# Performance work log

Measured on AMD Instinct MI355X. Metric: run time of the kernel, lower is better.

Reference implementation:

```python
import jax, jax.numpy as jnp
import numpy as np

B, N, H = 8, 2048, 256

def setup_inputs() -> dict:
    key = jax.random.key(0)
    k1, k2, k3, k4, k5 = jax.random.split(key, 5)
    h = jax.random.normal(k1, (B, N, H), dtype=jnp.float32)
    node_mask = jnp.ones((B, N, 1), dtype=jnp.float32)
    n_nodes = N  # unused by the forward math, kept for signature fidelity
    s1 = 1.0 / np.sqrt(H)
    W1 = jax.random.uniform(k2, (H, H), minval=-s1, maxval=s1, dtype=jnp.float32)
    b1 = jax.random.uniform(k3, (H,), minval=-s1, maxval=s1, dtype=jnp.float32)
    w2 = jax.random.uniform(k4, (H,), minval=-s1, maxval=s1, dtype=jnp.float32)
    b2 = jax.random.uniform(k5, (), minval=-s1, maxval=s1, dtype=jnp.float32)
    return {"h": h, "node_mask": node_mask, "n_nodes": n_nodes,
            "W1": W1, "b1": b1, "w2": w2, "b2": b2}

def reference(h, node_mask, n_nodes, W1, b1, w2, b2):
    # node_dec: Linear + SiLU
    x = jax.nn.silu(jnp.einsum('bnh,oh->bno', h, W1) + b1)  # [B,N,H]
    # pre_di applied to pairwise difference is linear, so factor:
    # pre_di(x_i - x_j) = (x_i @ w2) - (x_j @ w2) + b2
    s = jnp.einsum('bnh,h->bn', x, w2)                       # [B,N]
    out = s[:, :, None] - s[:, None, :] + b2                 # [B,N,N]
    return out.astype(jnp.int64)                             # torch .long() truncates
```

## Files before the change

kernel.cpp:

```cpp
#include <hip/hip_runtime.h>
#include <math.h>

#define B_ 8
#define N_ 2048
#define H_ 256

typedef double d4 __attribute__((ext_vector_type(4)));

__global__ __launch_bounds__(256)
void transpose_w1(const float* __restrict__ W1, float* __restrict__ W1T) {
    W1T[(size_t)blockIdx.x * H_ + threadIdx.x] =
        W1[(size_t)threadIdx.x * H_ + blockIdx.x];
}

__device__ __forceinline__ int self_probe_var() {
    const int l = threadIdx.x & 63;
    d4 z = {0.0, 0.0, 0.0, 0.0};
    d4 r1 = __builtin_amdgcn_mfma_f64_16x16x4f64((double)(l + 1), 1.0, z, 0, 0, 0);
    d4 r2 = __builtin_amdgcn_mfma_f64_16x16x4f64(1.0, (double)(l + 1), z, 0, 0, 0);
    d4 r3 = __builtin_amdgcn_mfma_f64_16x16x4f64((double)(l & 15), 1.0, z, 0, 0, 0);
    const double pw0 = __shfl(r1[0], 0, 64);
    const double pw1 = __shfl(r2[0], 0, 64);
    const double pw2 = __shfl(r3[0], 1, 64);
    const double pw3 = __shfl(r3[2], 16, 64);
    const double pw4 = __shfl(r2[2], 16, 64);
    if (pw0 != 100.0 || pw1 != 100.0) return 0;
    if (pw2 == 0.0 && pw3 == 24.0)  return 1;
    if (pw2 == 0.0 && pw3 == 36.0)  return 3;
    if (pw2 == 4.0 && pw4 == 124.0) return 2;
    if (pw2 == 4.0 && pw4 == 136.0) return 4;
    return 0;
}

__global__ __launch_bounds__(256)
__attribute__((amdgpu_waves_per_eu(2, 4)))
void s_mfma_uni(const float* __restrict__ hp, const float* __restrict__ W1T,
                const float* __restrict__ b1, const float* __restrict__ w2,
                double* __restrict__ s_out) {
    const int var = self_probe_var();
    if (var == 0) return;
    __shared__ float hs_t[H_][17];
    __shared__ double spart[4][16];
    const int t = threadIdx.x;
    const int lane = t & 63;
    const int wave = __builtin_amdgcn_readfirstlane(t >> 6);
    const int a15 = lane & 15, g = lane >> 4;
    const int m0 = blockIdx.x * 16;
    const int oc = wave * 64;

    #pragma unroll
    for (int i = 0; i < 16; ++i)
        hs_t[t][i] = hp[(size_t)(m0 + i) * H_ + t];
    __syncthreads();

    const float* bp = W1T + (size_t)g * H_ + oc + a15;

    d4 acc[4];
    #pragma unroll
    for (int ot = 0; ot < 4; ++ot) acc[ot] = (d4){0.0, 0.0, 0.0, 0.0};

    float ac[2], an[2];
    float bcv[8], bnv[8];
    ac[0] = hs_t[g][a15];
    ac[1] = hs_t[4 + g][a15];
    #pragma unroll
    for (int ot = 0; ot < 4; ++ot) {
        bcv[ot]     = bp[ot * 16];
        bcv[4 + ot] = bp[4 * H_ + ot * 16];
    }

    for (int kc = 0; kc < H_; kc += 8) {
        const int kn = (kc + 8 < H_) ? (kc + 8) : 0;
        an[0] = hs_t[kn + g][a15];
        an[1] = hs_t[kn + 4 + g][a15];
        #pragma unroll
        for (int ot = 0; ot < 4; ++ot) {
            bnv[ot]     = bp[(size_t)kn * H_ + ot * 16];
            bnv[4 + ot] = bp[(size_t)(kn + 4) * H_ + ot * 16];
        }
        {
            const double a0 = (double)ac[0];
            #pragma unroll
            for (int ot = 0; ot < 4; ++ot)
                acc[ot] = __builtin_amdgcn_mfma_f64_16x16x4f64(
                    a0, (double)bcv[ot], acc[ot], 0, 0, 0);
        }
        {
            const double a1 = (double)ac[1];
            #pragma unroll
            for (int ot = 0; ot < 4; ++ot)
                acc[ot] = __builtin_amdgcn_mfma_f64_16x16x4f64(
                    a1, (double)bcv[4 + ot], acc[ot], 0, 0, 0);
        }
        ac[0] = an[0]; ac[1] = an[1];
        #pragma unroll
        for (int q = 0; q < 8; ++q) bcv[q] = bnv[q];
    }

    if (var == 1 || var == 3) {
        double psum[4] = {0.0, 0.0, 0.0, 0.0};
        #pragma unroll
        for (int ot = 0; ot < 4; ++ot) {
            const int o = oc + ot * 16 + a15;
            const double bb = (double)b1[o];
            const double ww = (double)w2[o];
            #pragma unroll
            for (int v = 0; v < 4; ++v) {
                const double u = acc[ot][v] + bb;
                psum[v] += ww * (u / (1.0 + exp(-u)));
            }
        }
        #pragma unroll
        for (int v = 0; v < 4; ++v) {
            double x = psum[v];
            x += __shfl_xor(x, 1, 64);
            x += __shfl_xor(x, 2, 64);
            x += __shfl_xor(x, 4, 64);
            x += __shfl_xor(x, 8, 64);
            psum[v] = x;
        }
        if (a15 == 0) {
            #pragma unroll
            for (int v = 0; v < 4; ++v) {
                const int row = (var == 1) ? (4 * g + v) : (g + 4 * v);
                spart[wave][row] = psum[v];
            }
        }
    } else {
        double ps = 0.0;
        #pragma unroll
        for (int ot = 0; ot < 4; ++ot)
            #pragma unroll
            for (int v = 0; v < 4; ++v) {
                const int cv = (var == 2) ? (4 * g + v) : (g + 4 * v);
                const int o = oc + ot * 16 + cv;
                const double u = acc[ot][v] + (double)b1[o];
                ps += (double)w2[o] * (u / (1.0 + exp(-u)));
            }
        ps += __shfl_xor(ps, 16, 64);
        ps += __shfl_xor(ps, 32, 64);
        if (g == 0) spart[wave][a15] = ps;
    }
    __syncthreads();
    if (t < 16)
        s_out[m0 + t] = spart[0][t] + spart[1][t] + spart[2][t] + spart[3][t];
}

__global__ __launch_bounds__(256)
__attribute__((amdgpu_waves_per_eu(2, 4)))
void s_valu_kernel(const float* __restrict__ hp, const float* __restrict__ W1T,
                   const float* __restrict__ b1, const float* __restrict__ w2,
                   double* __restrict__ s_out) {
    if (self_probe_var() != 0) return;
    const int t = threadIdx.x;
    const int lane = t & 63;
    const int wave = __builtin_amdgcn_readfirstlane(t >> 6);
    const int m0 = blockIdx.x * 16 + wave * 4;
    const int o0 = lane * 4;
    const float* hr = hp + (size_t)m0 * H_;
    const float* wp = W1T + o0;

    double acc[4][4];
    #pragma unroll
    for (int j = 0; j < 4; ++j)
        #pragma unroll
        for (int r = 0; r < 4; ++r) acc[j][r] = 0.0;

    float4 wA[8], wB[8];
    float hA[32], hB[32];

    #define LOADW(dst, kcv)                                                   \
        do {                                                                  \
            _Pragma("unroll")                                                 \
            for (int kk = 0; kk < 8; ++kk)                                    \
                dst[kk] = *reinterpret_cast<const float4*>(                   \
                    wp + (size_t)((kcv) + kk) * H_);                          \
        } while (0)

    #define LOADH(dst, kcv)                                                   \
        do {                                                                  \
            _Pragma("unroll")                                                 \
            for (int r = 0; r < 4; ++r)                                       \
                _Pragma("unroll")                                             \
                for (int kk = 0; kk < 8; ++kk)                                \
                    dst[r * 8 + kk] = hr[r * H_ + (kcv) + kk];                \
        } while (0)

    #define COMPUTE(wv, hbuf)                                                 \
        do {                                                                  \
            _Pragma("unroll")                                                 \
            for (int kk = 0; kk < 8; ++kk) {                                  \
                const double h0 = (double)hbuf[0 * 8 + kk];                   \
                const double h1 = (double)hbuf[1 * 8 + kk];                   \
                const double h2 = (double)hbuf[2 * 8 + kk];                   \
                const double h3 = (double)hbuf[3 * 8 + kk];                   \
                const double a0 = (double)wv[kk].x;                           \
                const double a1 = (double)wv[kk].y;                           \
                const double a2 = (double)wv[kk].z;                           \
                const double a3 = (double)wv[kk].w;                           \
                acc[0][0] = fma(a0, h0, acc[0][0]);                           \
                acc[0][1] = fma(a0, h1, acc[0][1]);                           \
                acc[0][2] = fma(a0, h2, acc[0][2]);                           \
                acc[0][3] = fma(a0, h3, acc[0][3]);                           \
                acc[1][0] = fma(a1, h0, acc[1][0]);                           \
                acc[1][1] = fma(a1, h1, acc[1][1]);                           \
                acc[1][2] = fma(a1, h2, acc[1][2]);                           \
                acc[1][3] = fma(a1, h3, acc[1][3]);                           \
                acc[2][0] = fma(a2, h0, acc[2][0]);                           \
                acc[2][1] = fma(a2, h1, acc[2][1]);                           \
                acc[2][2] = fma(a2, h2, acc[2][2]);                           \
                acc[2][3] = fma(a2, h3, acc[2][3]);                           \
                acc[3][0] = fma(a3, h0, acc[3][0]);                           \
                acc[3][1] = fma(a3, h1, acc[3][1]);                           \
                acc[3][2] = fma(a3, h2, acc[3][2]);                           \
                acc[3][3] = fma(a3, h3, acc[3][3]);                           \
            }                                                                 \
        } while (0)

    LOADW(wA, 0);
    LOADH(hA, 0);
    for (int kc = 0; kc < H_; kc += 16) {
        LOADW(wB, kc + 8);
        LOADH(hB, kc + 8);
        COMPUTE(wA, hA);
        if (kc + 16 < H_) {
            LOADW(wA, kc + 16);
            LOADH(hA, kc + 16);
        }
        COMPUTE(wB, hB);
    }
    #undef LOADW
    #undef LOADH
    #undef COMPUTE

    const float4 b1v = *reinterpret_cast<const float4*>(b1 + o0);
    const float4 w2v = *reinterpret_cast<const float4*>(w2 + o0);
    double psum[4] = {0.0, 0.0, 0.0, 0.0};
    #define EPI(j, bc, wc)                                                    \
        do {                                                                  \
            const double bb = (double)bc, ww = (double)wc;                    \
            _Pragma("unroll")                                                 \
            for (int r = 0; r < 4; ++r) {                                     \
                const double u = acc[j][r] + bb;                              \
                psum[r] += ww * (u / (1.0 + exp(-u)));                        \
            }                                                                 \
        } while (0)
    EPI(0, b1v.x, w2v.x);
    EPI(1, b1v.y, w2v.y);
    EPI(2, b1v.z, w2v.z);
    EPI(3, b1v.w, w2v.w);
    #undef EPI

    #pragma unroll
    for (int r = 0; r < 4; ++r) {
        double v = psum[r];
        v += __shfl_xor(v, 1, 64);
        v += __shfl_xor(v, 2, 64);
        v += __shfl_xor(v, 4, 64);
        v += __shfl_xor(v, 8, 64);
        v += __shfl_xor(v, 16, 64);
        v += __shfl_xor(v, 32, 64);
        if (lane == 0) s_out[m0 + r] = v;
    }
}

__global__ __launch_bounds__(256)
void pair_kernel(const double* __restrict__ s, const float* __restrict__ b2p,
                 int* __restrict__ out) {
    const double b2 = (double)b2p[0];
    const unsigned total4 = (unsigned)(B_) * (unsigned)(N_) * (unsigned)(N_) / 4u;
    const unsigned stride = gridDim.x * blockDim.x;
    for (unsigned idx = blockIdx.x * blockDim.x + threadIdx.x; idx < total4;
         idx += stride) {
        const unsigned base = idx * 4u;
        const unsigned bi  = base >> 22;
        const unsigned rem = base & ((1u << 22) - 1u);
        const unsigned i   = rem >> 11;
        const unsigned j   = rem & (N_ - 1u);
        const double si = s[bi * N_ + i];
        const double* sp = s + bi * N_ + j;
        const double sj0 = sp[0], sj1 = sp[1], sj2 = sp[2], sj3 = sp[3];
        int4 o;
        o.x = (int)trunc((si - sj0) + b2);
        o.y = (int)trunc((si - sj1) + b2);
        o.z = (int)trunc((si - sj2) + b2);
        o.w = (int)trunc((si - sj3) + b2);
        *reinterpret_cast<int4*>(out + base) = o;
    }
}

extern "C" void kernel_launch(void* const* d_in, const int* in_sizes, int n_in,
                              void* d_out, int out_size, void* d_ws, size_t ws_size,
                              hipStream_t stream) {
    const float* hp = (const float*)d_in[0];
    const float* W1 = (const float*)d_in[3];
    const float* b1 = (const float*)d_in[4];
    const float* w2 = (const float*)d_in[5];
    const float* b2 = (const float*)d_in[6];

    float*  W1T = (float*)d_ws;
    double* s   = (double*)((char*)d_ws + 256 * 1024);
    int* out = (int*)d_out;

    transpose_w1<<<H_, H_, 0, stream>>>(W1, W1T);
    s_mfma_uni<<<(B_ * N_) / 16, 256, 0, stream>>>(hp, W1T, b1, w2, s);
    s_valu_kernel<<<(B_ * N_) / 16, 256, 0, stream>>>(hp, W1T, b1, w2, s);
    pair_kernel<<<2048, 256, 0, stream>>>(s, b2, out);
}
```

Before: 77.35 us.

## Merge MFMA and VALU s-kernels into one hybrid kernel splitting rows 5:3

Replaces the two separate s-computation kernels (MFMA path and VALU fallback) with a single kernel. When the MFMA probe succeeds, blocks are split so that 5 of every 8 run the FP64 MFMA path and 3 run the VALU FMA path, so matrix cores and vector ALUs work on different rows at the same time. This removes one kernel launch and tries to balance work across both execution units. The VALU blocks still allocate the MFMA path's shared memory, and the fixed 5:3 ratio may not match the two paths' relative throughput.

Result: slower. 104.2 us (+34.7%).

```diff
diff --git a/kernel.cpp b/kernel.cpp
--- a/kernel.cpp
+++ b/kernel.cpp
@@ -34,233 +34,237 @@
 
 __global__ __launch_bounds__(256)
 __attribute__((amdgpu_waves_per_eu(2, 4)))
-void s_mfma_uni(const float* __restrict__ hp, const float* __restrict__ W1T,
-                const float* __restrict__ b1, const float* __restrict__ w2,
-                double* __restrict__ s_out) {
-    const int var = self_probe_var();
-    if (var == 0) return;
+void s_hybrid(const float* __restrict__ hp, const float* __restrict__ W1T,
+              const float* __restrict__ b1, const float* __restrict__ w2,
+              double* __restrict__ s_out) {
     __shared__ float hs_t[H_][17];
     __shared__ double spart[4][16];
+    const int var = self_probe_var();
     const int t = threadIdx.x;
     const int lane = t & 63;
     const int wave = __builtin_amdgcn_readfirstlane(t >> 6);
-    const int a15 = lane & 15, g = lane >> 4;
-    const int m0 = blockIdx.x * 16;
-    const int oc = wave * 64;
-
-    #pragma unroll
-    for (int i = 0; i < 16; ++i)
-        hs_t[t][i] = hp[(size_t)(m0 + i) * H_ + t];
-    __syncthreads();
-
-    const float* bp = W1T + (size_t)g * H_ + oc + a15;
-
-    d4 acc[4];
-    #pragma unroll
-    for (int ot = 0; ot < 4; ++ot) acc[ot] = (d4){0.0, 0.0, 0.0, 0.0};
-
-    float ac[2], an[2];
-    float bcv[8], bnv[8];
-    ac[0] = hs_t[g][a15];
-    ac[1] = hs_t[4 + g][a15];
-    #pragma unroll
-    for (int ot = 0; ot < 4; ++ot) {
-        bcv[ot]     = bp[ot * 16];
-        bcv[4 + ot] = bp[4 * H_ + ot * 16];
+
+    int mfma_mode, m0;
+    if (var != 0) {
+        const int grp = blockIdx.x >> 3, slot = blockIdx.x & 7;
+        if (slot < 5) { mfma_mode = 1; m0 = (grp * 5 + slot) * 16; }
+        else          { mfma_mode = 0; m0 = (640 + grp * 3 + (slot - 5)) * 16; }
+    } else {
+        mfma_mode = 0;
+        m0 = blockIdx.x * 16;
     }
 
-    for (int kc = 0; kc < H_; kc += 8) {
-        const int kn = (kc + 8 < H_) ? (kc + 8) : 0;
-        an[0] = hs_t[kn + g][a15];
-        an[1] = hs_t[kn + 4 + g][a15];
+    if (mfma_mode) {
+        const int a15 = lane & 15, g = lane >> 4;
+        const int oc = wave * 64;
+
+        #pragma unroll
+        for (int i = 0; i < 16; ++i)
+            hs_t[t][i] = hp[(size_t)(m0 + i) * H_ + t];
+        __syncthreads();
+
+        const float* bp = W1T + (size_t)g * H_ + oc + a15;
+
+        d4 acc[4];
+        #pragma unroll
+        for (int ot = 0; ot < 4; ++ot) acc[ot] = (d4){0.0, 0.0, 0.0, 0.0};
+
+        float ac[2], an[2];
+        float bcv[8], bnv[8];
+        ac[0] = hs_t[g][a15];
+        ac[1] = hs_t[4 + g][a15];
         #pragma unroll
         for (int ot = 0; ot < 4; ++ot) {
-            bnv[ot]     = bp[(size_t)kn * H_ + ot * 16];
-            bnv[4 + ot] = bp[(size_t)(kn + 4) * H_ + ot * 16];
-        }
-        {
-            const double a0 = (double)ac[0];
+            bcv[ot]     = bp[ot * 16];
+            bcv[4 + ot] = bp[4 * H_ + ot * 16];
+        }
+
+        for (int kc = 0; kc < H_; kc += 8) {
+            const int kn = (kc + 8 < H_) ? (kc + 8) : 0;
+            an[0] = hs_t[kn + g][a15];
+            an[1] = hs_t[kn + 4 + g][a15];
+            #pragma unroll
+            for (int ot = 0; ot < 4; ++ot) {
+                bnv[ot]     = bp[(size_t)kn * H_ + ot * 16];
+                bnv[4 + ot] = bp[(size_t)(kn + 4) * H_ + ot * 16];
+            }
+            {
+                const double a0 = (double)ac[0];
+                #pragma unroll
+                for (int ot = 0; ot < 4; ++ot)
+                    acc[ot] = __builtin_amdgcn_mfma_f64_16x16x4f64(
+                        a0, (double)bcv[ot], acc[ot], 0, 0, 0);
+            }
+            {
+                const double a1 = (double)ac[1];
+                #pragma unroll
+                for (int ot = 0; ot < 4; ++ot)
+                    acc[ot] = __builtin_amdgcn_mfma_f64_16x16x4f64(
+                        a1, (double)bcv[4 + ot], acc[ot], 0, 0, 0);
+            }
+            ac[0] = an[0]; ac[1] = an[1];
+            #pragma unroll
+            for (int q = 0; q < 8; ++q) bcv[q] = bnv[q];
+        }
+
+        if (var == 1 || var == 3) {
+            double psum[4] = {0.0, 0.0, 0.0, 0.0};
+            #pragma unroll
+            for (int ot = 0; ot < 4; ++ot) {
+                const int o = oc + ot * 16 + a15;
+                const double bb = (double)b1[o];
+                const double ww = (double)w2[o];
+                #pragma unroll
+                for (int v = 0; v < 4; ++v) {
+                    const double u = acc[ot][v] + bb;
+                    psum[v] += ww * (u / (1.0 + exp(-u)));
+                }
+            }
+            #pragma unroll
+            for (int v = 0; v < 4; ++v) {
+                double x = psum[v];
+                x += __shfl_xor(x, 1, 64);
+                x += __shfl_xor(x, 2, 64);
+                x += __shfl_xor(x, 4, 64);
+                x += __shfl_xor(x, 8, 64);
+                psum[v] = x;
+            }
+            if (a15 == 0) {
+                #pragma unroll
+                for (int v = 0; v < 4; ++v) {
+                    const int row = (var == 1) ? (4 * g + v) : (g + 4 * v);
+                    spart[wave][row] = psum[v];
+                }
+            }
+        } else {
+            double ps = 0.0;
             #pragma unroll
             for (int ot = 0; ot < 4; ++ot)
-                acc[ot] = __builtin_amdgcn_mfma_f64_16x16x4f64(
-                    a0, (double)bcv[ot], acc[ot], 0, 0, 0);
-        }
-        {
-            const double a1 = (double)ac[1];
-            #pragma unroll
-            for (int ot = 0; ot < 4; ++ot)
-                acc[ot] = __builtin_amdgcn_mfma_f64_16x16x4f64(
-                    a1, (double)bcv[4 + ot], acc[ot], 0, 0, 0);
-        }
-        ac[0] = an[0]; ac[1] = an[1];
-        #pragma unroll
-        for (int q = 0; q < 8; ++q) bcv[q] = bnv[q];
+                #pragma unroll
+                for (int v = 0; v < 4; ++v) {
+                    const int cv = (var == 2) ? (4 * g + v) : (g + 4 * v);
+                    const int o = oc + ot * 16 + cv;
+                    const double u = acc[ot][v] + (double)b1[o];
+                    ps += (double)w2[o] * (u / (1.0 + exp(-u)));
+                }
+            ps += __shfl_xor(ps, 16, 64);
+            ps += __shfl_xor(ps, 32, 64);
+            if (g == 0) spart[wave][a15] = ps;
+        }
+        __syncthreads();
+        if (t < 16)
+            s_out[m0 + t] = spart[0][t] + spart[1][t] + spart[2][t] + spart[3][t];
+        return;
     }
 
-    if (var == 1 || var == 3) {
-        double psum[4] = {0.0, 0.0, 0.0, 0.0};
-        #pragma unroll
-        for (int ot = 0; ot < 4; ++ot) {
-            const int o = oc + ot * 16 + a15;
-            const double bb = (double)b1[o];
-            const double ww = (double)w2[o];
-            #pragma unroll
-            for (int v = 0; v < 4; ++v) {
-                const double u = acc[ot][v] + bb;
-                psum[v] += ww * (u / (1.0 + exp(-u)));
-            }
-        }
-        #pragma unroll
-        for (int v = 0; v < 4; ++v) {
-            double x = psum[v];
-            x += __shfl_xor(x, 1, 64);
-            x += __shfl_xor(x, 2, 64);
-            x += __shfl_xor(x, 4, 64);
-            x += __shfl_xor(x, 8, 64);
-            psum[v] = x;
-        }
-        if (a15 == 0) {
-            #pragma unroll
-            for (int v = 0; v < 4; ++v) {
-                const int row = (var == 1) ? (4 * g + v) : (g + 4 * v);
-                spart[wave][row] = psum[v];
-            }
-        }
-    } else {
-        double ps = 0.0;
-        #pragma unroll
-        for (int ot = 0; ot < 4; ++ot)
-            #pragma unroll
-            for (int v = 0; v < 4; ++v) {
-                const int cv = (var == 2) ? (4 * g + v) : (g + 4 * v);
-                const int o = oc + ot * 16 + cv;
-                const double u = acc[ot][v] + (double)b1[o];
-                ps += (double)w2[o] * (u / (1.0 + exp(-u)));
-            }
-        ps += __shfl_xor(ps, 16, 64);
-        ps += __shfl_xor(ps, 32, 64);
-        if (g == 0) spart[wave][a15] = ps;
-    }
-    __syncthreads();
-    if (t < 16)
-        s_out[m0 + t] = spart[0][t] + spart[1][t] + spart[2][t] + spart[3][t];
-}
-
-__global__ __launch_bounds__(256)
-__attribute__((amdgpu_waves_per_eu(2, 4)))
-void s_valu_kernel(const float* __restrict__ hp, const float* __restrict__ W1T,
-                   const float* __restrict__ b1, const float* __restrict__ w2,
-                   double* __restrict__ s_out) {
-    if (self_probe_var() != 0) return;
-    const int t = threadIdx.x;
-    const int lane = t & 63;
-    const int wave = __builtin_amdgcn_readfirstlane(t >> 6);
-    const int m0 = blockIdx.x * 16 + wave * 4;
-    const int o0 = lane * 4;
-    const float* hr = hp + (size_t)m0 * H_;
-    const float* wp = W1T + o0;
-
-    double acc[4][4];
-    #pragma unroll
-    for (int j = 0; j < 4; ++j)
-        #pragma unroll
-        for (int r = 0; r < 4; ++r) acc[j][r] = 0.0;
-
-    float4 wA[8], wB[8];
-    float hA[32], hB[32];
-
-    #define LOADW(dst, kcv)                                                   \
-        do {                                                                  \
-            _Pragma("unroll")                                                 \
-            for (int kk = 0; kk < 8; ++kk)                                    \
-                dst[kk] = *reinterpret_cast<const float4*>(                   \
-                    wp + (size_t)((kcv) + kk) * H_);                          \
-        } while (0)
-
-    #define LOADH(dst, kcv)                                                   \
-        do {                                                                  \
-            _Pragma("unroll")                                                 \
-            for (int r = 0; r < 4; ++r)                                       \
+    {
+        const int mv0 = m0 + wave * 4;
+        const int o0 = lane * 4;
+        const float* hr = hp + (size_t)mv0 * H_;
+        const float* wp = W1T + o0;
+
+        double acc[4][4];
+        #pragma unroll
+        for (int j = 0; j < 4; ++j)
+            #pragma unroll
+            for (int r = 0; r < 4; ++r) acc[j][r] = 0.0;
+
+        float4 wA[8], wB[8];
+        float hA[32], hB[32];
+
+        #define VLOADW(dst, kcv)                                              \
+            do {                                                              \
                 _Pragma("unroll")                                             \
                 for (int kk = 0; kk < 8; ++kk)                                \
-                    dst[r * 8 + kk] = hr[r * H_ + (kcv) + kk];                \
-        } while (0)
-
-    #define COMPUTE(wv, hbuf)                                                 \
-        do {                                                                  \
-            _Pragma("unroll")                                                 \
-            for (int kk = 0; kk < 8; ++kk) {                                  \
-                const double h0 = (double)hbuf[0 * 8 + kk];                   \
-                const double h1 = (double)hbuf[1 * 8 + kk];                   \
-                const double h2 = (double)hbuf[2 * 8 + kk];                   \
-                const double h3 = (double)hbuf[3 * 8 + kk];                   \
-                const double a0 = (double)wv[kk].x;                           \
-                const double a1 = (double)wv[kk].y;                           \
-                const double a2 = (double)wv[kk].z;                           \
-                const double a3 = (double)wv[kk].w;                           \
-                acc[0][0] = fma(a0, h0, acc[0][0]);                           \
-                acc[0][1] = fma(a0, h1, acc[0][1]);                           \
-                acc[0][2] = fma(a0, h2, acc[0][2]);                           \
-                acc[0][3] = fma(a0, h3, acc[0][3]);                           \
-                acc[1][0] = fma(a1, h0, acc[1][0]);                           \
-                acc[1][1] = fma(a1, h1, acc[1][1]);                           \
-                acc[1][2] = fma(a1, h2, acc[1][2]);                           \
-                acc[1][3] = fma(a1, h3, acc[1][3]);                           \
-                acc[2][0] = fma(a2, h0, acc[2][0]);                           \
-                acc[2][1] = fma(a2, h1, acc[2][1]);                           \
-                acc[2][2] = fma(a2, h2, acc[2][2]);                           \
-                acc[2][3] = fma(a2, h3, acc[2][3]);                           \
-                acc[3][0] = fma(a3, h0, acc[3][0]);                           \
-                acc[3][1] = fma(a3, h1, acc[3][1]);                           \
-                acc[3][2] = fma(a3, h2, acc[3][2]);                           \
-                acc[3][3] = fma(a3, h3, acc[3][3]);                           \
-            }                                                                 \
-        } while (0)
-
-    LOADW(wA, 0);
-    LOADH(hA, 0);
-    for (int kc = 0; kc < H_; kc += 16) {
-        LOADW(wB, kc + 8);
-        LOADH(hB, kc + 8);
-        COMPUTE(wA, hA);
-        if (kc + 16 < H_) {
-            LOADW(wA, kc + 16);
-            LOADH(hA, kc + 16);
-        }
-        COMPUTE(wB, hB);
-    }
-    #undef LOADW
-    #undef LOADH
-    #undef COMPUTE
-
-    const float4 b1v = *reinterpret_cast<const float4*>(b1 + o0);
-    const float4 w2v = *reinterpret_cast<const float4*>(w2 + o0);
-    double psum[4] = {0.0, 0.0, 0.0, 0.0};
-    #define EPI(j, bc, wc)                                                    \
-        do {                                                                  \
-            const double bb = (double)bc, ww = (double)wc;                    \
-            _Pragma("unroll")                                                 \
-            for (int r = 0; r < 4; ++r) {                                     \
-                const double u = acc[j][r] + bb;                              \
-                psum[r] += ww * (u / (1.0 + exp(-u)));                        \
-            }                                                                 \
-        } while (0)
-    EPI(0, b1v.x, w2v.x);
-    EPI(1, b1v.y, w2v.y);
-    EPI(2, b1v.z, w2v.z);
-    EPI(3, b1v.w, w2v.w);
-    #undef EPI
-
-    #pragma unroll
-    for (int r = 0; r < 4; ++r) {
-        double v = psum[r];
-        v += __shfl_xor(v, 1, 64);
-        v += __shfl_xor(v, 2, 64);
-        v += __shfl_xor(v, 4, 64);
-        v += __shfl_xor(v, 8, 64);
-        v += __shfl_xor(v, 16, 64);
-        v += __shfl_xor(v, 32, 64);
-        if (lane == 0) s_out[m0 + r] = v;
+                    dst[kk] = *reinterpret_cast<const float4*>(               \
+                        wp + (size_t)((kcv) + kk) * H_);                      \
+            } while (0)
+
+        #define VLOADH(dst, kcv)                                              \
+            do {                                                              \
+                _Pragma("unroll")                                             \
+                for (int r = 0; r < 4; ++r)                                   \
+                    _Pragma("unroll")                                         \
+                    for (int kk = 0; kk < 8; ++kk)                            \
+                        dst[r * 8 + kk] = hr[r * H_ + (kcv) + kk];            \
+            } while (0)
+
+        #define VCOMPUTE(wv, hbuf)                                            \
+            do {                                                              \
+                _Pragma("unroll")                                             \
+                for (int kk = 0; kk < 8; ++kk) {                              \
+                    const double h0 = (double)hbuf[0 * 8 + kk];               \
+                    const double h1 = (double)hbuf[1 * 8 + kk];               \
+                    const double h2 = (double)hbuf[2 * 8 + kk];               \
+                    const double h3 = (double)hbuf[3 * 8 + kk];               \
+                    const double a0 = (double)wv[kk].x;                       \
+                    const double a1 = (double)wv[kk].y;                       \
+                    const double a2 = (double)wv[kk].z;                       \
+                    const double a3 = (double)wv[kk].w;                       \
+                    acc[0][0] = fma(a0, h0, acc[0][0]);                       \
+                    acc[0][1] = fma(a0, h1, acc[0][1]);                       \
+                    acc[0][2] = fma(a0, h2, acc[0][2]);                       \
+                    acc[0][3] = fma(a0, h3, acc[0][3]);                       \
+                    acc[1][0] = fma(a1, h0, acc[1][0]);                       \
+                    acc[1][1] = fma(a1, h1, acc[1][1]);                       \
+                    acc[1][2] = fma(a1, h2, acc[1][2]);                       \
+                    acc[1][3] = fma(a1, h3, acc[1][3]);                       \
+                    acc[2][0] = fma(a2, h0, acc[2][0]);                       \
+                    acc[2][1] = fma(a2, h1, acc[2][1]);                       \
+                    acc[2][2] = fma(a2, h2, acc[2][2]);                       \
+                    acc[2][3] = fma(a2, h3, acc[2][3]);                       \
+                    acc[3][0] = fma(a3, h0, acc[3][0]);                       \
+                    acc[3][1] = fma(a3, h1, acc[3][1]);                       \
+                    acc[3][2] = fma(a3, h2, acc[3][2]);                       \
+                    acc[3][3] = fma(a3, h3, acc[3][3]);                       \
+                }                                                             \
+            } while (0)
+
+        VLOADW(wA, 0);
+        VLOADH(hA, 0);
+        for (int kc = 0; kc < H_; kc += 16) {
+            VLOADW(wB, kc + 8);
+            VLOADH(hB, kc + 8);
+            VCOMPUTE(wA, hA);
+            if (kc + 16 < H_) {
+                VLOADW(wA, kc + 16);
+                VLOADH(hA, kc + 16);
+            }
+            VCOMPUTE(wB, hB);
+        }
+        #undef VLOADW
+        #undef VLOADH
+        #undef VCOMPUTE
+
+        const float4 b1v = *reinterpret_cast<const float4*>(b1 + o0);
+        const float4 w2v = *reinterpret_cast<const float4*>(w2 + o0);
+        double psum[4] = {0.0, 0.0, 0.0, 0.0};
+        #define VEPI(j, bc, wc)                                               \
+            do {                                                              \
+                const double bb = (double)bc, ww = (double)wc;                \
+                _Pragma("unroll")                                             \
+                for (int r = 0; r < 4; ++r) {                                 \
+                    const double u = acc[j][r] + bb;                          \
+                    psum[r] += ww * (u / (1.0 + exp(-u)));                    \
+                }                                                             \
+            } while (0)
+        VEPI(0, b1v.x, w2v.x);
+        VEPI(1, b1v.y, w2v.y);
+        VEPI(2, b1v.z, w2v.z);
+        VEPI(3, b1v.w, w2v.w);
+        #undef VEPI
+
+        #pragma unroll
+        for (int r = 0; r < 4; ++r) {
+            double v = psum[r];
+            v += __shfl_xor(v, 1, 64);
+            v += __shfl_xor(v, 2, 64);
+            v += __shfl_xor(v, 4, 64);
+            v += __shfl_xor(v, 8, 64);
+            v += __shfl_xor(v, 16, 64);
+            v += __shfl_xor(v, 32, 64);
+            if (lane == 0) s_out[mv0 + r] = v;
+        }
     }
 }
 
@@ -303,7 +307,6 @@
     int* out = (int*)d_out;
 
     transpose_w1<<<H_, H_, 0, stream>>>(W1, W1T);
-    s_mfma_uni<<<(B_ * N_) / 16, 256, 0, stream>>>(hp, W1T, b1, w2, s);
-    s_valu_kernel<<<(B_ * N_) / 16, 256, 0, stream>>>(hp, W1T, b1, w2, s);
+    s_hybrid<<<(B_ * N_) / 16, 256, 0, stream>>>(hp, W1T, b1, w2, s);
     pair_kernel<<<2048, 256, 0, stream>>>(s, b2, out);
 }
```
